# Kernel optimization log

Hardware: AMD Instinct MI355X
Metric: run time of the kernel (lower is better)

Reference implementation:

```python
import jax, jax.numpy as jnp
import numpy as np

N_ATOMS = 100000
N_PAIRS = 3200000
N_PROP = 16
N_BASIS = 10
W = 16  # MLP width for pp/pi/ii nodes


def setup_inputs() -> dict:
    key = jax.random.key(0)
    ks = jax.random.split(key, 16)
    s = 0.1
    inp = {
        "ind_2": jax.random.randint(ks[0], (N_PAIRS, 2), 0, N_ATOMS),
        "p1": jax.random.normal(ks[1], (N_ATOMS, N_PROP), dtype=jnp.float32),
        "basis": jax.random.normal(ks[2], (N_PAIRS, N_BASIS), dtype=jnp.float32),
        # pp_pre: [16,16], bias=True
        "Wpre0": jax.random.normal(ks[3], (N_PROP, W), dtype=jnp.float32) * s,
        "bpre0": jnp.zeros((W,), dtype=jnp.float32),
        "Wpre1": jax.random.normal(ks[4], (W, W), dtype=jnp.float32) * s,
        "bpre1": jnp.zeros((W,), dtype=jnp.float32),
        # pi: input 2*W -> W -> W*n_basis, bias=True
        "Wpi0": jax.random.normal(ks[5], (2 * W, W), dtype=jnp.float32) * s,
        "bpi0": jnp.zeros((W,), dtype=jnp.float32),
        "Wpi1": jax.random.normal(ks[6], (W, W * N_BASIS), dtype=jnp.float32) * s,
        "bpi1": jnp.zeros((W * N_BASIS,), dtype=jnp.float32),
        # ii: [16,16], bias=False
        "Wii0": jax.random.normal(ks[7], (W, W), dtype=jnp.float32) * s,
        "Wii1": jax.random.normal(ks[8], (W, W), dtype=jnp.float32) * s,
        # pp_post: [16,16], bias=False
        "Wpost0": jax.random.normal(ks[9], (W, W), dtype=jnp.float32) * s,
        "Wpost1": jax.random.normal(ks[10], (W, W), dtype=jnp.float32) * s,
    }
    return inp


def reference(ind_2, p1, basis, Wpre0, bpre0, Wpre1, bpre1,
              Wpi0, bpi0, Wpi1, bpi1, Wii0, Wii1, Wpost0, Wpost1):
    act = jnp.tanh
    n_atoms = p1.shape[0]
    # pp_pre: per-atom FF (activation on every dense, bias=True)
    p1_in = act(p1 @ Wpre0 + bpre0)
    p1_in = act(p1_in @ Wpre1 + bpre1)
    # PI: gather pair endpoints, concat, MLP, contract with radial basis
    h = jnp.concatenate([p1_in[ind_2[:, 0]], p1_in[ind_2[:, 1]]], axis=-1)  # (P, 2W)
    h = act(h @ Wpi0 + bpi0)                                                # (P, W)
    h = act(h @ Wpi1 + bpi1)                                                # (P, W*n_basis)
    h = h.reshape(h.shape[0], -1, basis.shape[-1])                          # (P, W, n_basis)
    i_pair = jnp.einsum('pcb,pb->pc', h, basis)                             # (P, W)
    # II: pair-mixing FF (bias=False)
    i_pair = act(i_pair @ Wii0)
    i_pair = act(i_pair @ Wii1)
    # IP: scatter-sum pair features back to atoms at ind_2[:,0]
    p_sum = jax.ops.segment_sum(i_pair, ind_2[:, 0], num_segments=n_atoms)  # (A, W)
    # pp_post (bias=False)
    p1_new = act(p_sum @ Wpost0)
    p1_new = act(p1_new @ Wpost1)
    return (p1_new, i_pair)
```

## Files before the change

### kernel.cpp

```cpp
#include <hip/hip_runtime.h>

#define N_ATOMS 100000
#define N_PAIRS 3200000
#define N_PROP 16
#define N_BASIS 10
#define W 16
#define NT (N_PAIRS / 16)
#define NSUP (NT / 2)
#define SCAN_BLK 1024
#define NB ((N_ATOMS + SCAN_BLK - 1) / SCAN_BLK)
#define SC 2.88539008177792681f

typedef short  s16x8 __attribute__((ext_vector_type(8)));
typedef float  f32x4 __attribute__((ext_vector_type(4)));

__device__ __forceinline__ float tanh_pre(float y) {
    float e = __builtin_amdgcn_exp2f(y);
    return 1.0f - 2.0f * __builtin_amdgcn_rcpf(e + 1.0f);
}
__device__ __forceinline__ float fast_tanh(float x) {
    float e = __builtin_amdgcn_exp2f(x * SC);
    return 1.0f - 2.0f * __builtin_amdgcn_rcpf(e + 1.0f);
}
__device__ __forceinline__ unsigned short bf16r(float f) {
    union { float f; unsigned u; } v; v.f = f;
    unsigned r = v.u + 0x7FFFu + ((v.u >> 16) & 1u);
    return (unsigned short)(r >> 16);
}
__device__ __forceinline__ float bf16f(unsigned short h) {
    union { unsigned u; float f; } v; v.u = ((unsigned)h) << 16; return v.f;
}
__device__ __forceinline__ unsigned cvt_pk_bf16(float a, float b) {
    unsigned r;
    asm("v_cvt_pk_bf16_f32 %0, %1, %2" : "=v"(r) : "v"(a), "v"(b));
    return r;
}
__device__ __forceinline__ float bitf(unsigned u) {
    union { unsigned u; float f; } v; v.u = u; return v.f;
}

__global__ __launch_bounds__(256) void k_pp_pre(
    const float* __restrict__ p1,
    const float* __restrict__ W0, const float* __restrict__ b0,
    const float* __restrict__ W1, const float* __restrict__ b1,
    unsigned short* __restrict__ p1h, unsigned short* __restrict__ p1l)
{
    int a = blockIdx.x * 256 + threadIdx.x;
    if (a >= N_ATOMS) return;
    const float4* src = reinterpret_cast<const float4*>(p1 + (size_t)a * N_PROP);
    float4 v0 = src[0], v1 = src[1], v2 = src[2], v3 = src[3];
    float x[N_PROP] = {v0.x,v0.y,v0.z,v0.w, v1.x,v1.y,v1.z,v1.w,
                       v2.x,v2.y,v2.z,v2.w, v3.x,v3.y,v3.z,v3.w};
    float h[W];
#pragma unroll
    for (int c = 0; c < W; ++c) h[c] = b0[c];
#pragma unroll
    for (int k = 0; k < N_PROP; ++k)
#pragma unroll
        for (int c = 0; c < W; ++c) h[c] += x[k] * W0[k*W + c];
#pragma unroll
    for (int c = 0; c < W; ++c) h[c] = fast_tanh(h[c]);
    float y[W];
#pragma unroll
    for (int c = 0; c < W; ++c) y[c] = b1[c];
#pragma unroll
    for (int k = 0; k < W; ++k)
#pragma unroll
        for (int c = 0; c < W; ++c) y[c] += h[k] * W1[k*W + c];
    union { unsigned short u[8]; s16x8 v; } hi0, hi1, lo0, lo1;
#pragma unroll
    for (int c = 0; c < W; ++c) {
        float t = fast_tanh(y[c]);
        unsigned short hb = bf16r(t);
        unsigned short lb = bf16r(t - bf16f(hb));
        if (c < 8) { hi0.u[c] = hb; lo0.u[c] = lb; }
        else       { hi1.u[c-8] = hb; lo1.u[c-8] = lb; }
    }
    s16x8* dh = reinterpret_cast<s16x8*>(p1h + (size_t)a * W);
    s16x8* dl = reinterpret_cast<s16x8*>(p1l + (size_t)a * W);
    dh[0] = hi0.v; dh[1] = hi1.v;
    dl[0] = lo0.v; dl[1] = lo1.v;
}

__device__ __forceinline__ void make_B_hilo(const float x[4], int idxA, int idxB,
                                            int g, bool augment, s16x8& Bh, s16x8& Bl)
{
    unsigned w0h = cvt_pk_bf16(x[0], x[1]);
    unsigned w1h = cvt_pk_bf16(x[2], x[3]);
    float f0 = bitf(w0h << 16), f1 = bitf(w0h & 0xFFFF0000u);
    float f2 = bitf(w1h << 16), f3 = bitf(w1h & 0xFFFF0000u);
    unsigned w0l = cvt_pk_bf16(x[0] - f0, x[1] - f1);
    unsigned w1l = cvt_pk_bf16(x[2] - f2, x[3] - f3);
    union { unsigned u[4]; s16x8 v; } H, L;
    H.u[0] = (unsigned)__shfl((int)w0h, idxA); H.u[1] = (unsigned)__shfl((int)w1h, idxA);
    H.u[2] = (unsigned)__shfl((int)w0h, idxB); H.u[3] = (unsigned)__shfl((int)w1h, idxB);
    L.u[0] = (unsigned)__shfl((int)w0l, idxA); L.u[1] = (unsigned)__shfl((int)w1l, idxA);
    L.u[2] = (unsigned)__shfl((int)w0l, idxB); L.u[3] = (unsigned)__shfl((int)w1l, idxB);
    if (augment && g == 2) { H.u[0] = 0x3F80u; L.u[0] = 0u; }
    Bh = H.v; Bl = L.v;
}

__device__ __forceinline__ s16x8 make_B_hi(const float x[4], int idxA, int idxB)
{
    unsigned w0 = cvt_pk_bf16(x[0], x[1]);
    unsigned w1 = cvt_pk_bf16(x[2], x[3]);
    union { unsigned u[4]; s16x8 v; } H;
    H.u[0] = (unsigned)__shfl((int)w0, idxA); H.u[1] = (unsigned)__shfl((int)w1, idxA);
    H.u[2] = (unsigned)__shfl((int)w0, idxB); H.u[3] = (unsigned)__shfl((int)w1, idxB);
    return H.v;
}

template<int USE_RANK>
__global__ __launch_bounds__(256) void k_pair_mfma(
    const int*   __restrict__ ind2,
    const float* __restrict__ basis,
    const unsigned short* __restrict__ p1h,
    const unsigned short* __restrict__ p1l,
    const float* __restrict__ Wpi0, const float* __restrict__ bpi0,
    const float* __restrict__ Wpi1, const float* __restrict__ bpi1,
    const float* __restrict__ Wii0, const float* __restrict__ Wii1,
    float* __restrict__ i_pair_out,
    const unsigned* __restrict__ starts,
    const unsigned* __restrict__ rank,
    unsigned* __restrict__ cursor,
    float* __restrict__ svals)
{
    __shared__ s16x8 a2_lds[12][4][16];

    const int lane = threadIdx.x & 63;
    const int w    = threadIdx.x >> 6;
    const int r    = lane & 15;
    const int g    = lane >> 4;
    const int idxA = (r + 32*g) & 63;
    const int idxB = (idxA + 16) & 63;

    for (int e = threadIdx.x; e < 768; e += 256) {
        int t  = e >> 6;
        int rr = (e >> 2) & 15;
        int gg = e & 3;
        int ch = 4*(rr >> 2) + (t & 3);
        int bp = 4*(t >> 2) + (rr & 3);
        s16x8 val;
#pragma unroll
        for (int j = 0; j < 8; ++j) {
            int k = 8*gg + j;
            float wv = 0.0f;
            if (bp < N_BASIS) {
                if (k < W)       wv = Wpi1[k*(W*N_BASIS) + ch*N_BASIS + bp];
                else if (k == W) wv = bpi1[ch*N_BASIS + bp];
            }
            val[j] = (short)bf16r(SC * wv);
        }
        a2_lds[t][gg][rr] = val;
    }

    s16x8 a1, a3, a4;
#pragma unroll
    for (int j = 0; j < 8; ++j) {
        int k = 8*g + j;
        a1[j] = (short)bf16r(SC * Wpi0[k*W + r]);
        a3[j] = (short)(k < W ? bf16r(SC * Wii0[k*W + r]) : 0);
        a4[j] = (short)(k < W ? bf16r(SC * Wii1[k*W + r]) : 0);
    }
    float b0v[4];
#pragma unroll
    for (int i = 0; i < 4; ++i) b0v[i] = SC * bpi0[4*g + i];

    __syncthreads();

    for (int sup = blockIdx.x * 4 + w; sup < NSUP; sup += gridDim.x * 4) {
        const int pA = sup * 32 + r;
        const int pB = pA + 16;
        int2 ijA = reinterpret_cast<const int2*>(ind2)[pA];
        int2 ijB = reinterpret_cast<const int2*>(ind2)[pB];
        int atomA = (g < 2) ? ijA.x : ijA.y;
        int atomB = (g < 2) ? ijB.x : ijB.y;

        const s16x8 B1hA = *reinterpret_cast<const s16x8*>(p1h + (size_t)atomA * W + (g & 1) * 8);
        const s16x8 B1lA = *reinterpret_cast<const s16x8*>(p1l + (size_t)atomA * W + (g & 1) * 8);
        const s16x8 B1hB = *reinterpret_cast<const s16x8*>(p1h + (size_t)atomB * W + (g & 1) * 8);
        const s16x8 B1lB = *reinterpret_cast<const s16x8*>(p1l + (size_t)atomB * W + (g & 1) * 8);

        float basA[12], basB[12];
        {
            const float2* bbA = reinterpret_cast<const float2*>(basis + (size_t)pA * N_BASIS);
            const float2* bbB = reinterpret_cast<const float2*>(basis + (size_t)pB * N_BASIS);
#pragma unroll
            for (int q = 0; q < 5; ++q) {
                float2 tA = bbA[q]; basA[2*q] = tA.x; basA[2*q+1] = tA.y;
                float2 tB = bbB[q]; basB[2*q] = tB.x; basB[2*q+1] = tB.y;
            }
            basA[10] = basA[11] = 0.0f;
            basB[10] = basB[11] = 0.0f;
        }

        f32x4 accA = {0.f,0.f,0.f,0.f}, accB = {0.f,0.f,0.f,0.f};
        accA = __builtin_amdgcn_mfma_f32_16x16x32_bf16(a1, B1hA, accA, 0, 0, 0);
        accB = __builtin_amdgcn_mfma_f32_16x16x32_bf16(a1, B1hB, accB, 0, 0, 0);
        accA = __builtin_amdgcn_mfma_f32_16x16x32_bf16(a1, B1lA, accA, 0, 0, 0);
        accB = __builtin_amdgcn_mfma_f32_16x16x32_bf16(a1, B1lB, accB, 0, 0, 0);
        float h0A[4], h0B[4];
#pragma unroll
        for (int i = 0; i < 4; ++i) {
            h0A[i] = tanh_pre(accA[i] + b0v[i]);
            h0B[i] = tanh_pre(accB[i] + b0v[i]);
        }

        s16x8 B2hA, B2lA, B2hB, B2lB;
        make_B_hilo(h0A, idxA, idxB, g, true, B2hA, B2lA);
        make_B_hilo(h0B, idxA, idxB, g, true, B2hB, B2lB);

        float vlA[4] = {0.f,0.f,0.f,0.f}, vlB[4] = {0.f,0.f,0.f,0.f};
#pragma unroll
        for (int t = 0; t < 12; ++t) {
            s16x8 af = a2_lds[t][g][r];
            f32x4 zA = {0.f,0.f,0.f,0.f}, zB = {0.f,0.f,0.f,0.f};
            zA = __builtin_amdgcn_mfma_f32_16x16x32_bf16(af, B2hA, zA, 0, 0, 0);
            zB = __builtin_amdgcn_mfma_f32_16x16x32_bf16(af, B2hB, zB, 0, 0, 0);
            zA = __builtin_amdgcn_mfma_f32_16x16x32_bf16(af, B2lA, zA, 0, 0, 0);
            zB = __builtin_amdgcn_mfma_f32_16x16x32_bf16(af, B2lB, zB, 0, 0, 0);
#pragma unroll
            for (int i = 0; i < 4; ++i) {
                const int bi = 4*(t >> 2) + i;
                const int m  = t & 3;
                vlA[m] += tanh_pre(zA[i]) * basA[bi];
                vlB[m] += tanh_pre(zB[i]) * basB[bi];
            }
        }

        s16x8 B3hA = make_B_hi(vlA, idxA, idxB);
        s16x8 B3hB = make_B_hi(vlB, idxA, idxB);
        f32x4 uaA = {0.f,0.f,0.f,0.f}, uaB = {0.f,0.f,0.f,0.f};
        uaA = __builtin_amdgcn_mfma_f32_16x16x32_bf16(a3, B3hA, uaA, 0, 0, 0);
        uaB = __builtin_amdgcn_mfma_f32_16x16x32_bf16(a3, B3hB, uaB, 0, 0, 0);
        float tuA[4], tuB[4];
#pragma unroll
        for (int i = 0; i < 4; ++i) {
            tuA[i] = tanh_pre(uaA[i]);
            tuB[i] = tanh_pre(uaB[i]);
        }

        s16x8 B4hA = make_B_hi(tuA, idxA, idxB);
        s16x8 B4hB = make_B_hi(tuB, idxA, idxB);
        f32x4 waA = {0.f,0.f,0.f,0.f}, waB = {0.f,0.f,0.f,0.f};
        waA = __builtin_amdgcn_mfma_f32_16x16x32_bf16(a4, B4hA, waA, 0, 0, 0);
        waB = __builtin_amdgcn_mfma_f32_16x16x32_bf16(a4, B4hB, waB, 0, 0, 0);
        float4 outA = make_float4(tanh_pre(waA[0]), tanh_pre(waA[1]),
                                  tanh_pre(waA[2]), tanh_pre(waA[3]));
        float4 outB = make_float4(tanh_pre(waB[0]), tanh_pre(waB[1]),
                                  tanh_pre(waB[2]), tanh_pre(waB[3]));

        *reinterpret_cast<float4*>(i_pair_out + (size_t)pA * W + 4*g) = outA;
        *reinterpret_cast<float4*>(i_pair_out + (size_t)pB * W + 4*g) = outB;

        unsigned posA, posB;
        if (USE_RANK) {
            posA = starts[ijA.x] + rank[pA];
            posB = starts[ijB.x] + rank[pB];
        } else {
            unsigned ppA = 0, ppB = 0;
            if (g == 0) {
                ppA = atomicAdd(&cursor[ijA.x], 1u);
                ppB = atomicAdd(&cursor[ijB.x], 1u);
            }
            posA = (unsigned)__shfl((int)ppA, r);
            posB = (unsigned)__shfl((int)ppB, r);
        }
        *reinterpret_cast<float4*>(svals + (size_t)posA * W + 4*g) = outA;
        *reinterpret_cast<float4*>(svals + (size_t)posB * W + 4*g) = outB;
    }
}

__global__ __launch_bounds__(256) void k_count(const int* __restrict__ ind2,
                                               unsigned* __restrict__ counts,
                                               unsigned* __restrict__ rank)
{
    int p = blockIdx.x * 256 + threadIdx.x;
    if (p >= N_PAIRS) return;
    rank[p] = atomicAdd(&counts[ind2[2*p]], 1u);
}

__global__ __launch_bounds__(SCAN_BLK) void k_scanA(const unsigned* __restrict__ counts,
                                                    unsigned* __restrict__ starts,
                                                    unsigned* __restrict__ bsum)
{
    __shared__ unsigned sc[SCAN_BLK];
    int a = blockIdx.x * SCAN_BLK + threadIdx.x;
    unsigned c = (a < N_ATOMS) ? counts[a] : 0u;
    sc[threadIdx.x] = c;
    __syncthreads();
    for (int off = 1; off < SCAN_BLK; off <<= 1) {
        unsigned v = sc[threadIdx.x];
        unsigned add = (threadIdx.x >= off) ? sc[threadIdx.x - off] : 0u;
        __syncthreads();
        sc[threadIdx.x] = v + add;
        __syncthreads();
    }
    if (a < N_ATOMS) starts[a] = sc[threadIdx.x] - c;
    if (threadIdx.x == SCAN_BLK - 1) bsum[blockIdx.x] = sc[SCAN_BLK - 1];
}

__global__ __launch_bounds__(128) void k_scanB(const unsigned* __restrict__ bsum,
                                               unsigned* __restrict__ boff)
{
    __shared__ unsigned s[128];
    int t = threadIdx.x;
    unsigned v = (t < NB) ? bsum[t] : 0u;
    s[t] = v;
    __syncthreads();
    for (int off = 1; off < 128; off <<= 1) {
        unsigned x = s[t];
        unsigned add = (t >= off) ? s[t - off] : 0u;
        __syncthreads();
        s[t] = x + add;
        __syncthreads();
    }
    if (t < NB) boff[t] = s[t] - v;
}

__global__ __launch_bounds__(SCAN_BLK) void k_scanC(unsigned* __restrict__ starts,
                                                    const unsigned* __restrict__ boff,
                                                    unsigned* __restrict__ cursor)
{
    int a = blockIdx.x * SCAN_BLK + threadIdx.x;
    if (a >= N_ATOMS) return;
    unsigned s = starts[a] + boff[blockIdx.x];
    starts[a] = s;
    cursor[a] = s;
}

__global__ __launch_bounds__(256) void k_reduce_stream(const unsigned* __restrict__ starts,
                                                       const unsigned* __restrict__ counts,
                                                       const float* __restrict__ svals,
                                                       float* __restrict__ p_sum)
{
    int a = blockIdx.x * 4 + (threadIdx.x >> 6);
    if (a >= N_ATOMS) return;
    int lane = threadIdx.x & 63;
    int c = lane & 15, q = lane >> 4;
    unsigned n = counts[a], st = starts[a];
    float acc = 0.0f;
    for (unsigned k = q; k < n; k += 4)
        acc += svals[(size_t)(st + k) * W + c];
    acc += __shfl_xor(acc, 16);
    acc += __shfl_xor(acc, 32);
    if (q == 0) p_sum[(size_t)a * W + c] = acc;
}

__global__ __launch_bounds__(256) void k_pp_post(
    const float* __restrict__ p_sum,
    const float* __restrict__ W0, const float* __restrict__ W1,
    float* __restrict__ p1_new)
{
    int a = blockIdx.x * 256 + threadIdx.x;
    if (a >= N_ATOMS) return;
    const float4* src = reinterpret_cast<const float4*>(p_sum + (size_t)a * W);
    float4 v0 = src[0], v1 = src[1], v2 = src[2], v3 = src[3];
    float x[W] = {v0.x,v0.y,v0.z,v0.w, v1.x,v1.y,v1.z,v1.w,
                  v2.x,v2.y,v2.z,v2.w, v3.x,v3.y,v3.z,v3.w};
    float h[W];
#pragma unroll
    for (int c = 0; c < W; ++c) h[c] = 0.0f;
#pragma unroll
    for (int k = 0; k < W; ++k)
#pragma unroll
        for (int c = 0; c < W; ++c) h[c] += x[k] * W0[k*W + c];
#pragma unroll
    for (int c = 0; c < W; ++c) h[c] = fast_tanh(h[c]);
    float y[W];
#pragma unroll
    for (int c = 0; c < W; ++c) y[c] = 0.0f;
#pragma unroll
    for (int k = 0; k < W; ++k)
#pragma unroll
        for (int c = 0; c < W; ++c) y[c] += h[k] * W1[k*W + c];
    float4* dst = reinterpret_cast<float4*>(p1_new + (size_t)a * W);
    dst[0] = make_float4(fast_tanh(y[0]),  fast_tanh(y[1]),  fast_tanh(y[2]),  fast_tanh(y[3]));
    dst[1] = make_float4(fast_tanh(y[4]),  fast_tanh(y[5]),  fast_tanh(y[6]),  fast_tanh(y[7]));
    dst[2] = make_float4(fast_tanh(y[8]),  fast_tanh(y[9]),  fast_tanh(y[10]), fast_tanh(y[11]));
    dst[3] = make_float4(fast_tanh(y[12]), fast_tanh(y[13]), fast_tanh(y[14]), fast_tanh(y[15]));
}

extern "C" void kernel_launch(void* const* d_in, const int* in_sizes, int n_in,
                              void* d_out, int out_size, void* d_ws, size_t ws_size,
                              hipStream_t stream) {
    const int*   ind2   = (const int*)d_in[0];
    const float* p1     = (const float*)d_in[1];
    const float* basis  = (const float*)d_in[2];
    const float* Wpre0  = (const float*)d_in[3];
    const float* bpre0  = (const float*)d_in[4];
    const float* Wpre1  = (const float*)d_in[5];
    const float* bpre1  = (const float*)d_in[6];
    const float* Wpi0   = (const float*)d_in[7];
    const float* bpi0   = (const float*)d_in[8];
    const float* Wpi1   = (const float*)d_in[9];
    const float* bpi1   = (const float*)d_in[10];
    const float* Wii0   = (const float*)d_in[11];
    const float* Wii1   = (const float*)d_in[12];
    const float* Wpost0 = (const float*)d_in[13];
    const float* Wpost1 = (const float*)d_in[14];

    float* out    = (float*)d_out;
    float* p1_new = out;
    float* i_pair = out + (size_t)N_ATOMS * W;

    char* ws = (char*)d_ws;
    unsigned short* p1h = (unsigned short*)ws;                    ws += (size_t)N_ATOMS * W * 2;
    unsigned short* p1l = (unsigned short*)ws;                    ws += (size_t)N_ATOMS * W * 2;
    float*    p_sum  = (float*)ws;                                ws += (size_t)N_ATOMS * W * 4;
    unsigned* counts = (unsigned*)ws;                             ws += (size_t)N_ATOMS * 4;
    unsigned* starts = (unsigned*)ws;                             ws += (size_t)N_ATOMS * 4;
    unsigned* cursor = (unsigned*)ws;                             ws += (size_t)N_ATOMS * 4;
    unsigned* bsum   = (unsigned*)ws;                             ws += 1024 * 4;
    unsigned* boff   = (unsigned*)ws;                             ws += 1024 * 4;
    float*    svals  = (float*)ws;                                ws += (size_t)N_PAIRS * W * 4;
    unsigned* rank   = (unsigned*)ws;                             ws += (size_t)N_PAIRS * 4;

    int use_rank = (ws_size >= (size_t)(ws - (char*)d_ws));

    hipMemsetAsync(counts, 0, (size_t)N_ATOMS * sizeof(unsigned), stream);
    k_pp_pre<<<(N_ATOMS + 255) / 256, 256, 0, stream>>>(p1, Wpre0, bpre0, Wpre1, bpre1, p1h, p1l);
    k_count<<<(N_PAIRS + 255) / 256, 256, 0, stream>>>(ind2, counts, use_rank ? rank : cursor);
    k_scanA<<<NB, SCAN_BLK, 0, stream>>>(counts, starts, bsum);
    k_scanB<<<1, 128, 0, stream>>>(bsum, boff);
    k_scanC<<<NB, SCAN_BLK, 0, stream>>>(starts, boff, cursor);

    if (use_rank) {
        k_pair_mfma<1><<<2560, 256, 0, stream>>>(ind2, basis, p1h, p1l,
                                                 Wpi0, bpi0, Wpi1, bpi1, Wii0, Wii1,
                                                 i_pair, starts, rank, cursor, svals);
    } else {
        k_pair_mfma<0><<<2560, 256, 0, stream>>>(ind2, basis, p1h, p1l,
                                                 Wpi0, bpi0, Wpi1, bpi1, Wii0, Wii1,
                                                 i_pair, starts, rank, cursor, svals);
    }
    k_reduce_stream<<<(N_ATOMS + 3) / 4, 256, 0, stream>>>(starts, counts, svals, p_sum);
    k_pp_post<<<(N_ATOMS + 255) / 256, 256, 0, stream>>>(p_sum, Wpost0, Wpost1, p1_new);
}
```

Measured before the change: 584.9 us.

## Precompute per-atom first pair-layer halves and scatter pair indices instead of values

Result: slower. 735.4 us (+25.7%).

```diff
diff --git a/kernel.cpp b/kernel.cpp
--- a/kernel.cpp
+++ b/kernel.cpp
@@ -5,8 +5,7 @@
 #define N_PROP 16
 #define N_BASIS 10
 #define W 16
-#define NT (N_PAIRS / 16)
-#define NSUP (NT / 2)
+#define NSUP (N_PAIRS / 32)
 #define SCAN_BLK 1024
 #define NB ((N_ATOMS + SCAN_BLK - 1) / SCAN_BLK)
 #define SC 2.88539008177792681f
@@ -27,9 +26,6 @@
     unsigned r = v.u + 0x7FFFu + ((v.u >> 16) & 1u);
     return (unsigned short)(r >> 16);
 }
-__device__ __forceinline__ float bf16f(unsigned short h) {
-    union { unsigned u; float f; } v; v.u = ((unsigned)h) << 16; return v.f;
-}
 __device__ __forceinline__ unsigned cvt_pk_bf16(float a, float b) {
     unsigned r;
     asm("v_cvt_pk_bf16_f32 %0, %1, %2" : "=v"(r) : "v"(a), "v"(b));
@@ -43,7 +39,8 @@
     const float* __restrict__ p1,
     const float* __restrict__ W0, const float* __restrict__ b0,
     const float* __restrict__ W1, const float* __restrict__ b1,
-    unsigned short* __restrict__ p1h, unsigned short* __restrict__ p1l)
+    const float* __restrict__ Wpi0, const float* __restrict__ bpi0,
+    float* __restrict__ ytop, float* __restrict__ ybot)
 {
     int a = blockIdx.x * 256 + threadIdx.x;
     if (a >= N_ATOMS) return;
@@ -67,19 +64,27 @@
     for (int k = 0; k < W; ++k)
 #pragma unroll
         for (int c = 0; c < W; ++c) y[c] += h[k] * W1[k*W + c];
-    union { unsigned short u[8]; s16x8 v; } hi0, hi1, lo0, lo1;
-#pragma unroll
-    for (int c = 0; c < W; ++c) {
-        float t = fast_tanh(y[c]);
-        unsigned short hb = bf16r(t);
-        unsigned short lb = bf16r(t - bf16f(hb));
-        if (c < 8) { hi0.u[c] = hb; lo0.u[c] = lb; }
-        else       { hi1.u[c-8] = hb; lo1.u[c-8] = lb; }
-    }
-    s16x8* dh = reinterpret_cast<s16x8*>(p1h + (size_t)a * W);
-    s16x8* dl = reinterpret_cast<s16x8*>(p1l + (size_t)a * W);
-    dh[0] = hi0.v; dh[1] = hi1.v;
-    dl[0] = lo0.v; dl[1] = lo1.v;
+    float t[W];
+#pragma unroll
+    for (int c = 0; c < W; ++c) t[c] = fast_tanh(y[c]);
+
+    float yt[W], yb[W];
+#pragma unroll
+    for (int c = 0; c < W; ++c) { yt[c] = bpi0[c]; yb[c] = 0.0f; }
+#pragma unroll
+    for (int k = 0; k < W; ++k)
+#pragma unroll
+        for (int c = 0; c < W; ++c) {
+            yt[c] += t[k] * Wpi0[k*W + c];
+            yb[c] += t[k] * Wpi0[(W + k)*W + c];
+        }
+    float4* dt = reinterpret_cast<float4*>(ytop + (size_t)a * W);
+    float4* db = reinterpret_cast<float4*>(ybot + (size_t)a * W);
+#pragma unroll
+    for (int q = 0; q < 4; ++q) {
+        dt[q] = make_float4(SC*yt[4*q], SC*yt[4*q+1], SC*yt[4*q+2], SC*yt[4*q+3]);
+        db[q] = make_float4(SC*yb[4*q], SC*yb[4*q+1], SC*yb[4*q+2], SC*yb[4*q+3]);
+    }
 }
 
 __device__ __forceinline__ void make_B_hilo(const float x[4], int idxA, int idxB,
@@ -110,20 +115,17 @@
     return H.v;
 }
 
-template<int USE_RANK>
-__global__ __launch_bounds__(256) void k_pair_mfma(
+__global__ __launch_bounds__(256, 8) void k_pair_mfma(
     const int*   __restrict__ ind2,
     const float* __restrict__ basis,
-    const unsigned short* __restrict__ p1h,
-    const unsigned short* __restrict__ p1l,
-    const float* __restrict__ Wpi0, const float* __restrict__ bpi0,
+    const float* __restrict__ ytop,
+    const float* __restrict__ ybot,
     const float* __restrict__ Wpi1, const float* __restrict__ bpi1,
     const float* __restrict__ Wii0, const float* __restrict__ Wii1,
     float* __restrict__ i_pair_out,
     const unsigned* __restrict__ starts,
     const unsigned* __restrict__ rank,
-    unsigned* __restrict__ cursor,
-    float* __restrict__ svals)
+    unsigned* __restrict__ sidx)
 {
     __shared__ s16x8 a2_lds[12][4][16];
 
@@ -154,17 +156,13 @@
         a2_lds[t][gg][rr] = val;
     }
 
-    s16x8 a1, a3, a4;
+    s16x8 a3, a4;
 #pragma unroll
     for (int j = 0; j < 8; ++j) {
         int k = 8*g + j;
-        a1[j] = (short)bf16r(SC * Wpi0[k*W + r]);
         a3[j] = (short)(k < W ? bf16r(SC * Wii0[k*W + r]) : 0);
         a4[j] = (short)(k < W ? bf16r(SC * Wii1[k*W + r]) : 0);
     }
-    float b0v[4];
-#pragma unroll
-    for (int i = 0; i < 4; ++i) b0v[i] = SC * bpi0[4*g + i];
 
     __syncthreads();
 
@@ -173,15 +171,13 @@
         const int pB = pA + 16;
         int2 ijA = reinterpret_cast<const int2*>(ind2)[pA];
         int2 ijB = reinterpret_cast<const int2*>(ind2)[pB];
-        int atomA = (g < 2) ? ijA.x : ijA.y;
-        int atomB = (g < 2) ? ijB.x : ijB.y;
-
-        const s16x8 B1hA = *reinterpret_cast<const s16x8*>(p1h + (size_t)atomA * W + (g & 1) * 8);
-        const s16x8 B1lA = *reinterpret_cast<const s16x8*>(p1l + (size_t)atomA * W + (g & 1) * 8);
-        const s16x8 B1hB = *reinterpret_cast<const s16x8*>(p1h + (size_t)atomB * W + (g & 1) * 8);
-        const s16x8 B1lB = *reinterpret_cast<const s16x8*>(p1l + (size_t)atomB * W + (g & 1) * 8);
-
-        float basA[12], basB[12];
+
+        const f32x4 ytA = *reinterpret_cast<const f32x4*>(ytop + (size_t)ijA.x * W + 4*g);
+        const f32x4 ybA = *reinterpret_cast<const f32x4*>(ybot + (size_t)ijA.y * W + 4*g);
+        const f32x4 ytB = *reinterpret_cast<const f32x4*>(ytop + (size_t)ijB.x * W + 4*g);
+        const f32x4 ybB = *reinterpret_cast<const f32x4*>(ybot + (size_t)ijB.y * W + 4*g);
+
+        float basA[N_BASIS], basB[N_BASIS];
         {
             const float2* bbA = reinterpret_cast<const float2*>(basis + (size_t)pA * N_BASIS);
             const float2* bbB = reinterpret_cast<const float2*>(basis + (size_t)pB * N_BASIS);
@@ -190,20 +186,13 @@
                 float2 tA = bbA[q]; basA[2*q] = tA.x; basA[2*q+1] = tA.y;
                 float2 tB = bbB[q]; basB[2*q] = tB.x; basB[2*q+1] = tB.y;
             }
-            basA[10] = basA[11] = 0.0f;
-            basB[10] = basB[11] = 0.0f;
-        }
-
-        f32x4 accA = {0.f,0.f,0.f,0.f}, accB = {0.f,0.f,0.f,0.f};
-        accA = __builtin_amdgcn_mfma_f32_16x16x32_bf16(a1, B1hA, accA, 0, 0, 0);
-        accB = __builtin_amdgcn_mfma_f32_16x16x32_bf16(a1, B1hB, accB, 0, 0, 0);
-        accA = __builtin_amdgcn_mfma_f32_16x16x32_bf16(a1, B1lA, accA, 0, 0, 0);
-        accB = __builtin_amdgcn_mfma_f32_16x16x32_bf16(a1, B1lB, accB, 0, 0, 0);
+        }
+
         float h0A[4], h0B[4];
 #pragma unroll
         for (int i = 0; i < 4; ++i) {
-            h0A[i] = tanh_pre(accA[i] + b0v[i]);
-            h0B[i] = tanh_pre(accB[i] + b0v[i]);
+            h0A[i] = tanh_pre(ytA[i] + ybA[i]);
+            h0B[i] = tanh_pre(ytB[i] + ybB[i]);
         }
 
         s16x8 B2hA, B2lA, B2hB, B2lB;
@@ -222,9 +211,11 @@
 #pragma unroll
             for (int i = 0; i < 4; ++i) {
                 const int bi = 4*(t >> 2) + i;
-                const int m  = t & 3;
-                vlA[m] += tanh_pre(zA[i]) * basA[bi];
-                vlB[m] += tanh_pre(zB[i]) * basB[bi];
+                if (bi < N_BASIS) {
+                    const int m = t & 3;
+                    vlA[m] += tanh_pre(zA[i]) * basA[bi];
+                    vlB[m] += tanh_pre(zB[i]) * basB[bi];
+                }
             }
         }
 
@@ -253,21 +244,10 @@
         *reinterpret_cast<float4*>(i_pair_out + (size_t)pA * W + 4*g) = outA;
         *reinterpret_cast<float4*>(i_pair_out + (size_t)pB * W + 4*g) = outB;
 
-        unsigned posA, posB;
-        if (USE_RANK) {
-            posA = starts[ijA.x] + rank[pA];
-            posB = starts[ijB.x] + rank[pB];
-        } else {
-            unsigned ppA = 0, ppB = 0;
-            if (g == 0) {
-                ppA = atomicAdd(&cursor[ijA.x], 1u);
-                ppB = atomicAdd(&cursor[ijB.x], 1u);
-            }
-            posA = (unsigned)__shfl((int)ppA, r);
-            posB = (unsigned)__shfl((int)ppB, r);
-        }
-        *reinterpret_cast<float4*>(svals + (size_t)posA * W + 4*g) = outA;
-        *reinterpret_cast<float4*>(svals + (size_t)posB * W + 4*g) = outB;
+        if (g == 0) {
+            sidx[starts[ijA.x] + rank[pA]] = (unsigned)pA;
+            sidx[starts[ijB.x] + rank[pB]] = (unsigned)pB;
+        }
     }
 }
 
@@ -319,19 +299,17 @@
 }
 
 __global__ __launch_bounds__(SCAN_BLK) void k_scanC(unsigned* __restrict__ starts,
-                                                    const unsigned* __restrict__ boff,
-                                                    unsigned* __restrict__ cursor)
+                                                    const unsigned* __restrict__ boff)
 {
     int a = blockIdx.x * SCAN_BLK + threadIdx.x;
     if (a >= N_ATOMS) return;
-    unsigned s = starts[a] + boff[blockIdx.x];
-    starts[a] = s;
-    cursor[a] = s;
-}
-
-__global__ __launch_bounds__(256) void k_reduce_stream(const unsigned* __restrict__ starts,
+    starts[a] += boff[blockIdx.x];
+}
+
+__global__ __launch_bounds__(256) void k_reduce_gather(const unsigned* __restrict__ starts,
                                                        const unsigned* __restrict__ counts,
-                                                       const float* __restrict__ svals,
+                                                       const unsigned* __restrict__ sidx,
+                                                       const float* __restrict__ i_pair,
                                                        float* __restrict__ p_sum)
 {
     int a = blockIdx.x * 4 + (threadIdx.x >> 6);
@@ -340,8 +318,10 @@
     int c = lane & 15, q = lane >> 4;
     unsigned n = counts[a], st = starts[a];
     float acc = 0.0f;
-    for (unsigned k = q; k < n; k += 4)
-        acc += svals[(size_t)(st + k) * W + c];
+    for (unsigned k = q; k < n; k += 4) {
+        unsigned pid = sidx[st + k];
+        acc += i_pair[(size_t)pid * W + c];
+    }
     acc += __shfl_xor(acc, 16);
     acc += __shfl_xor(acc, 32);
     if (q == 0) p_sum[(size_t)a * W + c] = acc;
@@ -405,35 +385,27 @@
     float* i_pair = out + (size_t)N_ATOMS * W;
 
     char* ws = (char*)d_ws;
-    unsigned short* p1h = (unsigned short*)ws;                    ws += (size_t)N_ATOMS * W * 2;
-    unsigned short* p1l = (unsigned short*)ws;                    ws += (size_t)N_ATOMS * W * 2;
+    float*    ytop   = (float*)ws;                                ws += (size_t)N_ATOMS * W * 4;
+    float*    ybot   = (float*)ws;                                ws += (size_t)N_ATOMS * W * 4;
     float*    p_sum  = (float*)ws;                                ws += (size_t)N_ATOMS * W * 4;
     unsigned* counts = (unsigned*)ws;                             ws += (size_t)N_ATOMS * 4;
     unsigned* starts = (unsigned*)ws;                             ws += (size_t)N_ATOMS * 4;
-    unsigned* cursor = (unsigned*)ws;                             ws += (size_t)N_ATOMS * 4;
     unsigned* bsum   = (unsigned*)ws;                             ws += 1024 * 4;
     unsigned* boff   = (unsigned*)ws;                             ws += 1024 * 4;
-    float*    svals  = (float*)ws;                                ws += (size_t)N_PAIRS * W * 4;
     unsigned* rank   = (unsigned*)ws;                             ws += (size_t)N_PAIRS * 4;
-
-    int use_rank = (ws_size >= (size_t)(ws - (char*)d_ws));
+    unsigned* sidx   = (unsigned*)ws;                             ws += (size_t)N_PAIRS * 4;
 
     hipMemsetAsync(counts, 0, (size_t)N_ATOMS * sizeof(unsigned), stream);
-    k_pp_pre<<<(N_ATOMS + 255) / 256, 256, 0, stream>>>(p1, Wpre0, bpre0, Wpre1, bpre1, p1h, p1l);
-    k_count<<<(N_PAIRS + 255) / 256, 256, 0, stream>>>(ind2, counts, use_rank ? rank : cursor);
+    k_pp_pre<<<(N_ATOMS + 255) / 256, 256, 0, stream>>>(p1, Wpre0, bpre0, Wpre1, bpre1,
+                                                        Wpi0, bpi0, ytop, ybot);
+    k_count<<<(N_PAIRS + 255) / 256, 256, 0, stream>>>(ind2, counts, rank);
     k_scanA<<<NB, SCAN_BLK, 0, stream>>>(counts, starts, bsum);
     k_scanB<<<1, 128, 0, stream>>>(bsum, boff);
-    k_scanC<<<NB, SCAN_BLK, 0, stream>>>(starts, boff, cursor);
-
-    if (use_rank) {
-        k_pair_mfma<1><<<2560, 256, 0, stream>>>(ind2, basis, p1h, p1l,
-                                                 Wpi0, bpi0, Wpi1, bpi1, Wii0, Wii1,
-                                                 i_pair, starts, rank, cursor, svals);
-    } else {
-        k_pair_mfma<0><<<2560, 256, 0, stream>>>(ind2, basis, p1h, p1l,
-                                                 Wpi0, bpi0, Wpi1, bpi1, Wii0, Wii1,
-                                                 i_pair, starts, rank, cursor, svals);
-    }
-    k_reduce_stream<<<(N_ATOMS + 3) / 4, 256, 0, stream>>>(starts, counts, svals, p_sum);
+    k_scanC<<<NB, SCAN_BLK, 0, stream>>>(starts, boff);
+
+    k_pair_mfma<<<2048, 256, 0, stream>>>(ind2, basis, ytop, ybot,
+                                          Wpi1, bpi1, Wii0, Wii1,
+                                          i_pair, starts, rank, sidx);
+    k_reduce_gather<<<(N_ATOMS + 3) / 4, 256, 0, stream>>>(starts, counts, sidx, i_pair, p_sum);
     k_pp_post<<<(N_ATOMS + 255) / 256, 256, 0, stream>>>(p_sum, Wpost0, Wpost1, p1_new);
 }
```
